# Performance work log

Hardware: AMD Instinct MI355X
Metric: run time of the kernel (lower is better)

Reference implementation:

```python
import jax, jax.numpy as jnp
import numpy as np


def _scinol_new_p(p0, S2, G, eta, M, cond):
    # SCINOL effective-parameter computation (done under no_grad in torch)
    denom = jnp.sqrt(S2 + M * M)
    theta = jnp.clip(G / denom, -1.0, 1.0)
    upd = jnp.where(cond, theta / (2.0 * denom) * eta, 0.0)
    return p0 + jax.lax.stop_gradient(upd)


def _conv(x, w, b):
    y = jax.lax.conv_general_dilated(x, w, window_strides=(1, 1), padding='VALID',
                                     dimension_numbers=('NCHW', 'OIHW', 'NCHW'))
    return y + b[None, :, None, None]


def _maxpool2(x):
    return jax.lax.reduce_window(x, -jnp.inf, jax.lax.max, (1, 1, 2, 2), (1, 1, 2, 2), 'VALID')


def _scinol_conv(x, w0, wS2, wG, weta, wM, b0, bS2, bG, beta):
    # M-update: per-input-channel mean (over batch) of max-abs over H,W
    stat = jax.lax.stop_gradient(jnp.mean(jnp.max(jnp.abs(x), axis=(2, 3)), axis=0))  # (C_in,)
    M = jnp.maximum(stat, wM)  # (C_in,)
    w = _scinol_new_p(w0, wS2, wG, weta, M[None, :, None, None], wG != 0)
    b = _scinol_new_p(b0, bS2, bG, beta, jnp.float32(1.0), bG != 0)
    return _conv(x, w, b)


def _scinol_linear(x, w0, wS2, wG, weta, wM, b0, bS2, bG, beta):
    stat = jax.lax.stop_gradient(jnp.mean(jnp.abs(x), axis=0))  # (in_features,)
    M = jnp.maximum(wM, stat)  # broadcast -> (out, in)
    w = _scinol_new_p(w0, wS2, wG, weta, M, wS2 != 0)
    b = _scinol_new_p(b0, bS2, bG, beta, jnp.float32(1.0), bS2 != 0)
    return x @ w.T + b


def setup_inputs() -> dict:
    key = jax.random.key(0)
    ks = iter(jax.random.split(key, 40))
    f32 = jnp.float32
    d = {}
    d['x'] = jax.random.normal(next(ks), (2048, 1, 28, 28), dtype=f32)
    for pre, wshape, cin in [('c1', (64, 1, 5, 5), 1), ('c2', (64, 64, 5, 5), 64)]:
        d[pre + '_w0'] = jax.random.normal(next(ks), wshape, dtype=f32) * 0.1
        d[pre + '_wS2'] = jax.random.uniform(next(ks), wshape, dtype=f32)
        d[pre + '_wG'] = jax.random.normal(next(ks), wshape, dtype=f32)
        d[pre + '_weta'] = jax.random.uniform(next(ks), wshape, dtype=f32)
        d[pre + '_wM'] = jax.random.uniform(next(ks), (cin,), dtype=f32)
        d[pre + '_b0'] = jax.random.normal(next(ks), (64,), dtype=f32) * 0.1
        d[pre + '_bS2'] = jax.random.uniform(next(ks), (64,), dtype=f32)
        d[pre + '_bG'] = jax.random.normal(next(ks), (64,), dtype=f32)
        d[pre + '_beta'] = jax.random.uniform(next(ks), (64,), dtype=f32)
    d['l_w0'] = jax.random.normal(next(ks), (10, 1024), dtype=f32) * 0.03
    d['l_wS2'] = jax.random.uniform(next(ks), (10, 1024), dtype=f32)
    d['l_wG'] = jax.random.normal(next(ks), (10, 1024), dtype=f32)
    d['l_weta'] = jax.random.uniform(next(ks), (10, 1024), dtype=f32)
    d['l_wM'] = jax.random.uniform(next(ks), (10, 1024), dtype=f32)
    d['l_b0'] = jax.random.normal(next(ks), (10,), dtype=f32) * 0.03
    d['l_bS2'] = jax.random.uniform(next(ks), (10,), dtype=f32)
    d['l_bG'] = jax.random.normal(next(ks), (10,), dtype=f32)
    d['l_beta'] = jax.random.uniform(next(ks), (10,), dtype=f32)
    return d


def reference(x,
              c1_w0, c1_wS2, c1_wG, c1_weta, c1_wM, c1_b0, c1_bS2, c1_bG, c1_beta,
              c2_w0, c2_wS2, c2_wG, c2_weta, c2_wM, c2_b0, c2_bS2, c2_bG, c2_beta,
              l_w0, l_wS2, l_wG, l_weta, l_wM, l_b0, l_bS2, l_bG, l_beta):
    h = _scinol_conv(x, c1_w0, c1_wS2, c1_wG, c1_weta, c1_wM, c1_b0, c1_bS2, c1_bG, c1_beta)
    h = _maxpool2(jax.nn.relu(h))                      # (N,64,12,12)
    h = _scinol_conv(h, c2_w0, c2_wS2, c2_wG, c2_weta, c2_wM, c2_b0, c2_bS2, c2_bG, c2_beta)
    h = _maxpool2(jax.nn.relu(h))                      # (N,64,4,4)
    h = h.reshape(h.shape[0], -1)                      # (N,1024)
    return _scinol_linear(h, l_w0, l_wS2, l_wG, l_weta, l_wM, l_b0, l_bS2, l_bG, l_beta)
```

## Files before the change

### kernel.cpp

```cpp
#include <hip/hip_runtime.h>
#include <hip/hip_bf16.h>

typedef float v4f __attribute__((ext_vector_type(4)));
typedef short v8s __attribute__((ext_vector_type(8)));

#define WS_STAT2   0
#define WS_STATL   64
#define WS_B1      1088
#define WS_B2      1152
#define WS_WL      1216
#define WS_BL      11456
#define WS_IMAX    11520
#define WS_W1F_B   54272
#define WS_WP2_B   62464
#define WS_P1_B    267264
#define WS_P2_B    38016000
#define WS_C1MAX_F 9504000
#define WS_LPART_F 66816

__global__ void k_stat1(const float* __restrict__ x, float* ws) {
    int tid = threadIdx.x;
    int wv = tid >> 6, lane = tid & 63;
    int n = blockIdx.x * 4 + wv;
    const float* p = x + n * 784;
    float m = 0.f;
    for (int i = lane; i < 784; i += 64) m = fmaxf(m, fabsf(p[i]));
#pragma unroll
    for (int off = 32; off; off >>= 1) m = fmaxf(m, __shfl_xor(m, off, 64));
    if (lane == 0) ws[WS_IMAX + n] = m;
}

__global__ void k_prepw1(const float* __restrict__ w0, const float* __restrict__ S2,
                         const float* __restrict__ G, const float* __restrict__ eta,
                         const float* __restrict__ wM,
                         const float* __restrict__ b0, const float* __restrict__ bS2,
                         const float* __restrict__ bG, const float* __restrict__ beta,
                         float* ws) {
    __shared__ float red[256];
    int tid = threadIdx.x;
    float p = 0.f;
    for (int i = tid; i < 2048; i += 256) p += ws[WS_IMAX + i];
    red[tid] = p;
    __syncthreads();
    for (int s = 128; s > 0; s >>= 1) {
        if (tid < s) red[tid] += red[tid + s];
        __syncthreads();
    }
    float M = fmaxf(red[0] * (1.f / 2048.f), wM[0]);

    int i = blockIdx.x * 256 + tid;
    if (i < 4096) {
        int j = i & 7, m16 = (i >> 3) & 15, q = (i >> 7) & 3, ot = i >> 9;
        int tap = q * 8 + j, oc = m16 * 4 + ot;
        float v = 0.f;
        if (tap < 25) {
            int s = oc * 25 + tap;
            float g = G[s];
            float den = sqrtf(S2[s] + M * M);
            float inv = 1.f / den;
            float th = fminf(fmaxf(g * inv, -1.f), 1.f);
            v = w0[s] + ((g != 0.f) ? th * 0.5f * inv * eta[s] : 0.f);
        }
        ((__hip_bfloat16*)((char*)ws + WS_W1F_B))[i] = __float2bfloat16(v);
    } else if (i < 4160) {
        int c = i - 4096;
        float g = bG[c];
        float den = sqrtf(bS2[c] + 1.f);
        float inv = 1.f / den;
        float th = fminf(fmaxf(g * inv, -1.f), 1.f);
        ws[WS_B1 + c] = b0[c] + ((g != 0.f) ? th * 0.5f * inv * beta[c] : 0.f);
    }
}

__global__ void __launch_bounds__(256)
k_conv1(const float* __restrict__ x, float* ws, __hip_bfloat16* __restrict__ pool1) {
    __shared__ __align__(16) ushort sXh[1024];
    __shared__ int sMax[64];
    int n = blockIdx.x, tid = threadIdx.x;
    int wv = tid >> 6, lane = tid & 63;
    int m16 = lane & 15, quad = lane >> 4;

    {
        const float4* src = (const float4*)(x + (size_t)n * 784);
        float4 v = {0.f, 0.f, 0.f, 0.f};
        if (tid < 196) v = src[tid];
        ushort4 h;
        h.x = __bfloat16_as_ushort(__float2bfloat16(v.x));
        h.y = __bfloat16_as_ushort(__float2bfloat16(v.y));
        h.z = __bfloat16_as_ushort(__float2bfloat16(v.z));
        h.w = __bfloat16_as_ushort(__float2bfloat16(v.w));
        ((ushort4*)sXh)[tid] = h;
    }
    if (tid < 64) sMax[tid] = 0;

    const ushort* wfrag = (const ushort*)((const char*)ws + WS_W1F_B);
    v8s bfr[4];
#pragma unroll
    for (int ot = 0; ot < 4; ++ot)
        bfr[ot] = *(const v8s*)(wfrag + ((ot * 4 + quad) * 16 + m16) * 8);
    float4 bias = *(const float4*)(ws + WS_B1 + m16 * 4);

    int dj[8];
#pragma unroll
    for (int j = 0; j < 8; ++j) {
        int tap = quad * 8 + j;
        int u = (tap * 13) >> 6;
        dj[j] = tap + 23 * u;
    }

    int W0 = wv * 36 + (m16 >> 2);
    int wy = (W0 * 171) >> 11;
    int wx = W0 - wy * 12;
    int coff = 28 * ((m16 >> 1) & 1) + (m16 & 1);

    __syncthreads();

    float vmax[4] = {0.f, 0.f, 0.f, 0.f};
    ushort* op = (ushort*)(pool1 + (size_t)n * 9216);

    ushort g[8];
    {
        int base = 56 * wy + 2 * wx + coff;
#pragma unroll
        for (int j = 0; j < 8; ++j) g[j] = sXh[base + dj[j]];
    }
    for (int mt = 0; mt < 9; ++mt) {
        union { v8s v; ushort us[8]; } ua;
#pragma unroll
        for (int j = 0; j < 8; ++j) ua.us[j] = g[j];

        wx += 4;
        if (wx >= 12) { wx -= 12; ++wy; }
        if (mt < 8) {
            int nb = 56 * wy + 2 * wx + coff;
#pragma unroll
            for (int j = 0; j < 8; ++j) g[j] = sXh[nb + dj[j]];
        }

        v4f z = {0.f, 0.f, 0.f, 0.f};
        v4f acc[4];
#pragma unroll
        for (int ot = 0; ot < 4; ++ot)
            acc[ot] = __builtin_amdgcn_mfma_f32_16x16x32_bf16(ua.v, bfr[ot], z, 0, 0, 0);

        int Wd = (wv * 9 + mt) * 4 + quad;
        ushort4 pk;
#pragma unroll
        for (int ot = 0; ot < 4; ++ot) {
            v4f a = acc[ot];
            float m = fmaxf(fmaxf(a[0], a[1]), fmaxf(a[2], a[3]));
            float pv = fmaxf(m + bias[ot], 0.f);
            vmax[ot] = fmaxf(vmax[ot], pv);
            ((ushort*)&pk)[ot] = __bfloat16_as_ushort(__float2bfloat16(pv));
        }
        *(ushort4*)(op + Wd * 64 + m16 * 4) = pk;
    }

#pragma unroll
    for (int ot = 0; ot < 4; ++ot) {
        float m = vmax[ot];
        m = fmaxf(m, __shfl_xor(m, 16, 64));
        m = fmaxf(m, __shfl_xor(m, 32, 64));
        if (lane < 16) atomicMax(&sMax[lane * 4 + ot], __float_as_int(m));
    }
    __syncthreads();
    if (tid < 64) ws[WS_C1MAX_F + n * 64 + tid] = __int_as_float(sMax[tid]);
}

__global__ void k_stat2red(float* ws) {
    __shared__ float red[256];
    int c = blockIdx.x, t = threadIdx.x;
    float s = 0.f;
    for (int n = t; n < 2048; n += 256) s += ws[WS_C1MAX_F + n * 64 + c];
    red[t] = s;
    __syncthreads();
    for (int k = 128; k > 0; k >>= 1) {
        if (t < k) red[t] += red[t + k];
        __syncthreads();
    }
    if (t == 0) ws[WS_STAT2 + c] = red[0] * (1.f / 2048.f);
}

__global__ void k_prepw2(const float* __restrict__ w0, const float* __restrict__ S2,
                         const float* __restrict__ G, const float* __restrict__ eta,
                         const float* __restrict__ wM,
                         const float* __restrict__ b0, const float* __restrict__ bS2,
                         const float* __restrict__ bG, const float* __restrict__ beta,
                         float* ws, __hip_bfloat16* __restrict__ wp2) {
    int i = blockIdx.x * 256 + threadIdx.x;
    int j = i & 7, m16 = (i >> 3) & 15, quad = (i >> 7) & 3;
    int ot = (i >> 9) & 3, kc = (i >> 11) & 1, uv = i >> 12;
    int oc = ot * 16 + m16, ic = kc * 32 + quad * 8 + j;
    int s = oc * 1600 + ic * 25 + uv;
    float M = fmaxf(ws[WS_STAT2 + ic], wM[ic]);
    float g = G[s];
    float den = sqrtf(S2[s] + M * M);
    float inv = 1.f / den;
    float th = fminf(fmaxf(g * inv, -1.f), 1.f);
    float v = w0[s] + ((g != 0.f) ? th * 0.5f * inv * eta[s] : 0.f);
    wp2[i] = __float2bfloat16(v);
    if (blockIdx.x == 0 && threadIdx.x < 64) {
        int c = threadIdx.x;
        float gb = bG[c];
        float den2 = sqrtf(bS2[c] + 1.f);
        float inv2 = 1.f / den2;
        float th2 = fminf(fmaxf(gb * inv2, -1.f), 1.f);
        ws[WS_B2 + c] = b0[c] + ((gb != 0.f) ? th2 * 0.5f * inv2 * beta[c] : 0.f);
    }
}

__global__ void __launch_bounds__(256, 2)
k_conv2(const ushort* __restrict__ pool1, const ushort* __restrict__ wp2,
        const float* __restrict__ ws, float* __restrict__ pool2) {
    __shared__ __align__(16) ushort sImg[4 * 9216];
    __shared__ __align__(16) ushort sB[4096];
    int tid = threadIdx.x;
    int wv = tid >> 6, lane = tid & 63;
    int n0 = blockIdx.x * 4;

    {
        const uint4* src = (const uint4*)(pool1 + (size_t)n0 * 9216);
        uint4* dst = (uint4*)sImg;
#pragma unroll
        for (int img = 0; img < 4; ++img) {
            int b = img * 1152;
#pragma unroll
            for (int i = 0; i < 4; ++i) {
                int c = tid + i * 256;
                int r = c >> 3, col = c & 7;
                dst[b + r * 8 + (col ^ (r & 7))] = src[b + c];
            }
            if (tid < 128) {
                int c = 1024 + tid;
                int r = c >> 3, col = c & 7;
                dst[b + r * 8 + (col ^ (r & 7))] = src[b + c];
            }
        }
    }

    int m16 = lane & 15, quad = lane >> 4;
    int x0 = m16 & 7;
    int yb = m16 >> 3;
    int rbase = yb * 12 + x0;

    v4f acc[4][4];
#pragma unroll
    for (int i = 0; i < 4; ++i)
#pragma unroll
        for (int j = 0; j < 4; ++j) acc[i][j] = (v4f){0.f, 0.f, 0.f, 0.f};

    const uint4* bsrc = (const uint4*)wp2;
    uint4 br0 = bsrc[tid], br1 = bsrc[256 + tid];

    __syncthreads();
    ((uint4*)sB)[tid] = br0;
    ((uint4*)sB)[256 + tid] = br1;
    __syncthreads();

    const ushort* simg = sImg + wv * 9216;

    for (int uv = 0; uv < 25; ++uv) {
        uint4 nr0, nr1;
        if (uv < 24) {
            const uint4* nb = bsrc + (uv + 1) * 512;
            nr0 = nb[tid];
            nr1 = nb[256 + tid];
        }
        int u = (uv * 13) >> 6;
        int v = uv - u * 5;
        int r0_ = rbase + u * 12 + v;
#pragma unroll
        for (int kc = 0; kc < 2; ++kc) {
            v8s pA[4], pB[4];
#pragma unroll
            for (int pt = 0; pt < 4; ++pt) {
                int row = r0_ + pt * 24;
                int rs = row & 7;
                pA[pt] = *(const v8s*)(simg + row * 64 + (((kc * 4 + quad) ^ rs) << 3));
            }
#pragma unroll
            for (int ot = 0; ot < 4; ++ot)
                pB[ot] = *(const v8s*)(sB + (kc * 4 + ot) * 512 + lane * 8);
#pragma unroll
            for (int pt = 0; pt < 4; ++pt)
#pragma unroll
                for (int ot = 0; ot < 4; ++ot)
                    acc[pt][ot] = __builtin_amdgcn_mfma_f32_16x16x32_bf16(
                        pA[pt], pB[ot], acc[pt][ot], 0, 0, 0);
        }
        if (uv < 24) {
            __syncthreads();
            ((uint4*)sB)[tid] = nr0;
            ((uint4*)sB)[256 + tid] = nr1;
            __syncthreads();
        }
    }

    int n = n0 + wv;
    float bv[4];
#pragma unroll
    for (int ot = 0; ot < 4; ++ot) bv[ot] = ws[WS_B2 + ot * 16 + m16];
    float* outp = pool2 + (size_t)n * 1024;
#pragma unroll
    for (int pt = 0; pt < 4; ++pt)
#pragma unroll
        for (int ot = 0; ot < 4; ++ot) {
            v4f a = acc[pt][ot];
            float m01 = fmaxf(a[0], a[1]);
            float m23 = fmaxf(a[2], a[3]);
            m01 = fmaxf(m01, __shfl_xor(m01, 32, 64));
            m23 = fmaxf(m23, __shfl_xor(m23, 32, 64));
            if (lane < 32) {
                int oc = ot * 16 + m16;
                int f = oc * 16 + pt * 4 + (quad & 1) * 2;
                outp[f] = fmaxf(m01 + bv[ot], 0.f);
                outp[f + 1] = fmaxf(m23 + bv[ot], 0.f);
            }
        }
}

__global__ void k_statl(const float* __restrict__ pool2, float* ws) {
    int b = blockIdx.x, tid = threadIdx.x;
    float4 s = {0.f, 0.f, 0.f, 0.f};
    for (int im = 0; im < 32; ++im) {
        float4 v = ((const float4*)(pool2 + (size_t)(b * 32 + im) * 1024))[tid];
        s.x += v.x; s.y += v.y; s.z += v.z; s.w += v.w;
    }
    ((float4*)(ws + WS_LPART_F + b * 1024))[tid] = s;
}

__global__ void k_prepwl(const float* __restrict__ w0, const float* __restrict__ S2,
                         const float* __restrict__ G, const float* __restrict__ eta,
                         const float* __restrict__ wM,
                         const float* __restrict__ b0, const float* __restrict__ bS2,
                         const float* __restrict__ bG, const float* __restrict__ beta,
                         float* ws) {
    int i = blockIdx.x * 256 + threadIdx.x;
    if (i < 10240) {
        int f = i & 1023;
        float s = 0.f;
#pragma unroll
        for (int b = 0; b < 64; ++b) s += ws[WS_LPART_F + b * 1024 + f];
        float stat = s * (1.f / 2048.f);
        float M = fmaxf(wM[i], stat);
        float s2 = S2[i];
        float den = sqrtf(s2 + M * M);
        float inv = 1.f / den;
        float th = fminf(fmaxf(G[i] * inv, -1.f), 1.f);
        ws[WS_WL + i] = w0[i] + ((s2 != 0.f) ? th * 0.5f * inv * eta[i] : 0.f);
    } else if (i < 10250) {
        int c = i - 10240;
        float s2 = bS2[c];
        float den = sqrtf(s2 + 1.f);
        float inv = 1.f / den;
        float th = fminf(fmaxf(bG[c] * inv, -1.f), 1.f);
        ws[WS_BL + c] = b0[c] + ((s2 != 0.f) ? th * 0.5f * inv * beta[c] : 0.f);
    }
}

__global__ void k_linear(const float* __restrict__ pool2, const float* __restrict__ ws,
                         float* __restrict__ out) {
    int tid = threadIdx.x;
    int wv = tid >> 6, lane = tid & 63;
    int n = blockIdx.x * 4 + wv;
    const float* hp = pool2 + (size_t)n * 1024;
    float h[16];
#pragma unroll
    for (int j = 0; j < 16; ++j) h[j] = hp[j * 64 + lane];
    for (int oc = 0; oc < 10; ++oc) {
        const float* wp = ws + WS_WL + oc * 1024;
        float d = 0.f;
#pragma unroll
        for (int j = 0; j < 16; ++j) d = fmaf(h[j], wp[j * 64 + lane], d);
#pragma unroll
        for (int off = 32; off; off >>= 1) d += __shfl_xor(d, off, 64);
        if (lane == 0) out[n * 10 + oc] = d + ws[WS_BL + oc];
    }
}

extern "C" void kernel_launch(void* const* d_in, const int* in_sizes, int n_in,
                              void* d_out, int out_size, void* d_ws, size_t ws_size,
                              hipStream_t stream) {
    const float* x = (const float*)d_in[0];
    float* ws = (float*)d_ws;
    __hip_bfloat16* wp2 = (__hip_bfloat16*)((char*)d_ws + WS_WP2_B);
    __hip_bfloat16* p1 = (__hip_bfloat16*)((char*)d_ws + WS_P1_B);
    float* p2 = (float*)((char*)d_ws + WS_P2_B);
    float* out = (float*)d_out;

    k_stat1<<<512, 256, 0, stream>>>(x, ws);
    k_prepw1<<<17, 256, 0, stream>>>(
        (const float*)d_in[1], (const float*)d_in[2], (const float*)d_in[3],
        (const float*)d_in[4], (const float*)d_in[5], (const float*)d_in[6],
        (const float*)d_in[7], (const float*)d_in[8], (const float*)d_in[9], ws);
    k_conv1<<<2048, 256, 0, stream>>>(x, ws, p1);
    k_stat2red<<<64, 256, 0, stream>>>(ws);
    k_prepw2<<<400, 256, 0, stream>>>(
        (const float*)d_in[10], (const float*)d_in[11], (const float*)d_in[12],
        (const float*)d_in[13], (const float*)d_in[14], (const float*)d_in[15],
        (const float*)d_in[16], (const float*)d_in[17], (const float*)d_in[18], ws, wp2);
    k_conv2<<<512, 256, 0, stream>>>((const ushort*)p1, (const ushort*)wp2, ws, p2);
    k_statl<<<64, 256, 0, stream>>>(p2, ws);
    k_prepwl<<<41, 256, 0, stream>>>(
        (const float*)d_in[19], (const float*)d_in[20], (const float*)d_in[21],
        (const float*)d_in[22], (const float*)d_in[23], (const float*)d_in[24],
        (const float*)d_in[25], (const float*)d_in[26], (const float*)d_in[27], ws);
    k_linear<<<512, 256, 0, stream>>>(p2, ws, out);
}
```

Baseline: 197.8 us.

## Split conv2 K across wave pairs, 3 images per block, double-buffer weights

Restructures conv2 so each block handles 3 images with 6 waves. Each pair of waves splits the input-channel dimension of one image, and the two partial accumulators are combined through shared memory before the bias/ReLU/pool epilogue. The weight slice is now double-buffered in LDS, which cuts the per-tap barriers from two to one. The intent is more waves per image and less sync stall, at the cost of an extra LDS reduction, a tail block with a partial image count, and different occupancy limits.

```diff
diff --git a/kernel.cpp b/kernel.cpp
--- a/kernel.cpp
+++ b/kernel.cpp
@@ -209,39 +209,41 @@
     }
 }
 
-__global__ void __launch_bounds__(256, 2)
+__global__ void __launch_bounds__(384, 3)
 k_conv2(const ushort* __restrict__ pool1, const ushort* __restrict__ wp2,
         const float* __restrict__ ws, float* __restrict__ pool2) {
-    __shared__ __align__(16) ushort sImg[4 * 9216];
-    __shared__ __align__(16) ushort sB[4096];
+    __shared__ __align__(16) ushort sImg[3 * 9216];
+    __shared__ __align__(16) ushort sB[2][4096];
     int tid = threadIdx.x;
     int wv = tid >> 6, lane = tid & 63;
-    int n0 = blockIdx.x * 4;
+    int n0 = blockIdx.x * 3;
+    int nimg = min(3, 2048 - n0);
 
     {
         const uint4* src = (const uint4*)(pool1 + (size_t)n0 * 9216);
         uint4* dst = (uint4*)sImg;
 #pragma unroll
-        for (int img = 0; img < 4; ++img) {
-            int b = img * 1152;
-#pragma unroll
-            for (int i = 0; i < 4; ++i) {
-                int c = tid + i * 256;
-                int r = c >> 3, col = c & 7;
-                dst[b + r * 8 + (col ^ (r & 7))] = src[b + c];
-            }
-            if (tid < 128) {
-                int c = 1024 + tid;
-                int r = c >> 3, col = c & 7;
-                dst[b + r * 8 + (col ^ (r & 7))] = src[b + c];
-            }
-        }
+        for (int i = 0; i < 9; ++i) {
+            int c = tid + i * 384;
+            int img = c / 1152;
+            int w = c - img * 1152;
+            int r = w >> 3, col = w & 7;
+            if (img < nimg)
+                dst[img * 1152 + r * 8 + (col ^ (r & 7))] = src[c];
+        }
+    }
+    const uint4* bsrc = (const uint4*)wp2;
+    {
+        ((uint4*)sB[0])[tid] = bsrc[tid];
+        if (tid < 128) ((uint4*)sB[0])[384 + tid] = bsrc[384 + tid];
     }
 
     int m16 = lane & 15, quad = lane >> 4;
-    int x0 = m16 & 7;
-    int yb = m16 >> 3;
+    int x0 = m16 & 7, yb = m16 >> 3;
     int rbase = yb * 12 + x0;
+    int img_l = wv >> 1, kc = wv & 1;
+    int img_e = (img_l < nimg) ? img_l : 0;
+    const ushort* simg = sImg + img_e * 9216;
 
     v4f acc[4][4];
 #pragma unroll
@@ -249,74 +251,85 @@
 #pragma unroll
         for (int j = 0; j < 4; ++j) acc[i][j] = (v4f){0.f, 0.f, 0.f, 0.f};
 
-    const uint4* bsrc = (const uint4*)wp2;
-    uint4 br0 = bsrc[tid], br1 = bsrc[256 + tid];
-
-    __syncthreads();
-    ((uint4*)sB)[tid] = br0;
-    ((uint4*)sB)[256 + tid] = br1;
-    __syncthreads();
-
-    const ushort* simg = sImg + wv * 9216;
-
+    __syncthreads();
+
+    int cur = 0;
     for (int uv = 0; uv < 25; ++uv) {
         uint4 nr0, nr1;
         if (uv < 24) {
             const uint4* nb = bsrc + (uv + 1) * 512;
             nr0 = nb[tid];
-            nr1 = nb[256 + tid];
+            if (tid < 128) nr1 = nb[384 + tid];
         }
         int u = (uv * 13) >> 6;
         int v = uv - u * 5;
-        int r0_ = rbase + u * 12 + v;
-#pragma unroll
-        for (int kc = 0; kc < 2; ++kc) {
-            v8s pA[4], pB[4];
-#pragma unroll
-            for (int pt = 0; pt < 4; ++pt) {
-                int row = r0_ + pt * 24;
-                int rs = row & 7;
-                pA[pt] = *(const v8s*)(simg + row * 64 + (((kc * 4 + quad) ^ rs) << 3));
+        int r0 = rbase + u * 12 + v;
+
+        v8s pA[4], pB[4];
+#pragma unroll
+        for (int pt = 0; pt < 4; ++pt) {
+            int row = r0 + pt * 24;
+            int rs = row & 7;
+            pA[pt] = *(const v8s*)(simg + row * 64 + (((kc * 4 + quad) ^ rs) << 3));
+        }
+#pragma unroll
+        for (int ot = 0; ot < 4; ++ot)
+            pB[ot] = *(const v8s*)(sB[cur] + (kc * 4 + ot) * 512 + lane * 8);
+#pragma unroll
+        for (int pt = 0; pt < 4; ++pt)
+#pragma unroll
+            for (int ot = 0; ot < 4; ++ot)
+                acc[pt][ot] = __builtin_amdgcn_mfma_f32_16x16x32_bf16(
+                    pA[pt], pB[ot], acc[pt][ot], 0, 0, 0);
+
+        if (uv < 24) {
+            ((uint4*)sB[cur ^ 1])[tid] = nr0;
+            if (tid < 128) ((uint4*)sB[cur ^ 1])[384 + tid] = nr1;
+        }
+        __syncthreads();
+        cur ^= 1;
+    }
+
+    float* ex = (float*)sImg;
+    if (kc == 0 && img_l < nimg) {
+#pragma unroll
+        for (int pt = 0; pt < 4; ++pt)
+#pragma unroll
+            for (int ot = 0; ot < 4; ++ot)
+                *(v4f*)(ex + img_l * 4096 + (pt * 4 + ot) * 256 + lane * 4) = acc[pt][ot];
+    }
+    __syncthreads();
+    if (kc == 1 && img_l < nimg) {
+#pragma unroll
+        for (int pt = 0; pt < 4; ++pt)
+#pragma unroll
+            for (int ot = 0; ot < 4; ++ot) {
+                v4f p = *(const v4f*)(ex + img_l * 4096 + (pt * 4 + ot) * 256 + lane * 4);
+                acc[pt][ot] += p;
             }
-#pragma unroll
-            for (int ot = 0; ot < 4; ++ot)
-                pB[ot] = *(const v8s*)(sB + (kc * 4 + ot) * 512 + lane * 8);
-#pragma unroll
-            for (int pt = 0; pt < 4; ++pt)
-#pragma unroll
-                for (int ot = 0; ot < 4; ++ot)
-                    acc[pt][ot] = __builtin_amdgcn_mfma_f32_16x16x32_bf16(
-                        pA[pt], pB[ot], acc[pt][ot], 0, 0, 0);
-        }
-        if (uv < 24) {
-            __syncthreads();
-            ((uint4*)sB)[tid] = nr0;
-            ((uint4*)sB)[256 + tid] = nr1;
-            __syncthreads();
-        }
-    }
-
-    int n = n0 + wv;
-    float bv[4];
-#pragma unroll
-    for (int ot = 0; ot < 4; ++ot) bv[ot] = ws[WS_B2 + ot * 16 + m16];
-    float* outp = pool2 + (size_t)n * 1024;
-#pragma unroll
-    for (int pt = 0; pt < 4; ++pt)
-#pragma unroll
-        for (int ot = 0; ot < 4; ++ot) {
-            v4f a = acc[pt][ot];
-            float m01 = fmaxf(a[0], a[1]);
-            float m23 = fmaxf(a[2], a[3]);
-            m01 = fmaxf(m01, __shfl_xor(m01, 32, 64));
-            m23 = fmaxf(m23, __shfl_xor(m23, 32, 64));
-            if (lane < 32) {
-                int oc = ot * 16 + m16;
-                int f = oc * 16 + pt * 4 + (quad & 1) * 2;
-                outp[f] = fmaxf(m01 + bv[ot], 0.f);
-                outp[f + 1] = fmaxf(m23 + bv[ot], 0.f);
+
+        int n = n0 + img_l;
+        float bv[4];
+#pragma unroll
+        for (int ot = 0; ot < 4; ++ot) bv[ot] = ws[WS_B2 + ot * 16 + m16];
+        float* outp = pool2 + (size_t)n * 1024;
+#pragma unroll
+        for (int pt = 0; pt < 4; ++pt)
+#pragma unroll
+            for (int ot = 0; ot < 4; ++ot) {
+                v4f a = acc[pt][ot];
+                float m01 = fmaxf(a[0], a[1]);
+                float m23 = fmaxf(a[2], a[3]);
+                m01 = fmaxf(m01, __shfl_xor(m01, 32, 64));
+                m23 = fmaxf(m23, __shfl_xor(m23, 32, 64));
+                if (lane < 32) {
+                    int oc = ot * 16 + m16;
+                    int f = oc * 16 + pt * 4 + (quad & 1) * 2;
+                    outp[f] = fmaxf(m01 + bv[ot], 0.f);
+                    outp[f + 1] = fmaxf(m23 + bv[ot], 0.f);
+                }
             }
-        }
+    }
 }
 
 __global__ void k_statl(const float* __restrict__ pool2, float* ws) {
@@ -399,7 +412,7 @@
         (const float*)d_in[10], (const float*)d_in[11], (const float*)d_in[12],
         (const float*)d_in[13], (const float*)d_in[14], (const float*)d_in[15],
         (const float*)d_in[16], (const float*)d_in[17], (const float*)d_in[18], ws, wp2);
-    k_conv2<<<512, 256, 0, stream>>>((const ushort*)p1, (const ushort*)wp2, ws, p2);
+    k_conv2<<<683, 384, 0, stream>>>((const ushort*)p1, (const ushort*)wp2, ws, p2);
     k_statl<<<64, 256, 0, stream>>>(p2, ws);
     k_prepwl<<<41, 256, 0, stream>>>(
         (const float*)d_in[19], (const float*)d_in[20], (const float*)d_in[21],
```

Result: slower. 221.5 us (+11.9%).
